# Optimization experiments

Hardware: AMD Instinct MI355X
Metric: run time of the kernel (lower is better)

Reference implementation:

```python
import jax, jax.numpy as jnp
import numpy as np
from jax import lax

D_IN, HIDDEN, B, T = 64, 512, 256, 256


def _lstm_layer(x, W_ih, W_hh, b_ih, b_hh):
    """PyTorch-convention LSTM layer. x: [B, T, in]. Returns (ys [B,T,H], h_last [B,H]).
    Gate order i, f, g, o; gates = x W_ih^T + h W_hh^T + b_ih + b_hh."""
    Bb = x.shape[0]
    H = W_hh.shape[1]
    # precompute input projection for all timesteps: [T, B, 4H]
    xg = jnp.einsum('bti,gi->tbg', x, W_ih) + (b_ih + b_hh)
    h0 = jnp.zeros((Bb, H), dtype=x.dtype)
    c0 = jnp.zeros((Bb, H), dtype=x.dtype)

    def step(carry, xg_t):
        h, c = carry
        gates = xg_t + h @ W_hh.T  # [B, 4H]
        i, f, g, o = jnp.split(gates, 4, axis=-1)
        i = jax.nn.sigmoid(i)
        f = jax.nn.sigmoid(f)
        g = jnp.tanh(g)
        o = jax.nn.sigmoid(o)
        c = f * c + i * g
        h = o * jnp.tanh(c)
        return (h, c), h

    (h_last, _), ys = lax.scan(step, (h0, c0), xg)
    return ys.transpose(1, 0, 2), h_last


def setup_inputs() -> dict:
    key = jax.random.key(0)
    ks = jax.random.split(key, 12)
    s0 = 1.0 / np.sqrt(HIDDEN)  # PyTorch default init scale
    u = lambda k, shp: jax.random.uniform(k, shp, jnp.float32, -s0, s0)
    return {
        'x': jax.random.normal(ks[0], (B, T, D_IN), jnp.float32),
        'W_ih0': u(ks[1], (4 * HIDDEN, D_IN)),
        'W_hh0': u(ks[2], (4 * HIDDEN, HIDDEN)),
        'b_ih0': u(ks[3], (4 * HIDDEN,)),
        'b_hh0': u(ks[4], (4 * HIDDEN,)),
        'W_ih1': u(ks[5], (4 * HIDDEN, HIDDEN)),
        'W_hh1': u(ks[6], (4 * HIDDEN, HIDDEN)),
        'b_ih1': u(ks[7], (4 * HIDDEN,)),
        'b_hh1': u(ks[8], (4 * HIDDEN,)),
        'head_w': u(ks[9], (1, HIDDEN)),
        'head_b': u(ks[10], (1,)),
    }


def reference(x, W_ih0, W_hh0, b_ih0, b_hh0, W_ih1, W_hh1, b_ih1, b_hh1, head_w, head_b):
    ys0, _ = _lstm_layer(x, W_ih0, W_hh0, b_ih0, b_hh0)          # [B, T, H]
    _, h_last = _lstm_layer(ys0, W_ih1, W_hh1, b_ih1, b_hh1)    # only last step used
    out = h_last @ head_w.T + head_b                              # [B, 1]
    return out[:, 0]                                              # squeeze(-1) -> [B]
```

## Files before the change

### kernel.cpp

```cpp
#include <hip/hip_runtime.h>

#define HID 512
#define NB  256
#define TT  256
#define DIN 64
#define HBUF 131072
#define SLOT_SH HBUF
#define NSLOT 8

typedef __attribute__((ext_vector_type(8))) short short8;
typedef __attribute__((ext_vector_type(4))) float f32x4;

__device__ __forceinline__ unsigned short f2bf(float f) {
    unsigned int u = __float_as_uint(f);
    u += 0x7FFF + ((u >> 16) & 1);
    return (unsigned short)(u >> 16);
}
__device__ __forceinline__ float bf2f(unsigned short h) {
    return __uint_as_float(((unsigned int)h) << 16);
}

__device__ __forceinline__ float fsig(float x) {
    return __builtin_amdgcn_rcpf(1.f + __expf(-x));
}
__device__ __forceinline__ float ftanh(float x) {
    return 1.f - 2.f * __builtin_amdgcn_rcpf(1.f + __expf(2.f * x));
}

__device__ __forceinline__ void st_u32_llc(unsigned* p, unsigned v) {
    asm volatile("global_store_dword %0, %1, off sc0 sc1" :: "v"(p), "v"(v) : "memory");
}
__device__ __forceinline__ unsigned ld_u32_llc(const unsigned* p) {
    unsigned v;
    asm volatile("global_load_dword %0, %1, off sc0 sc1\n\ts_waitcnt vmcnt(0)"
                 : "=v"(v) : "v"(p) : "memory");
    return v;
}

#define MFMA2(acc, a, bh, bl)                                               \
    acc = __builtin_amdgcn_mfma_f32_16x16x32_bf16(a, bh, acc, 0, 0, 0);     \
    acc = __builtin_amdgcn_mfma_f32_16x16x32_bf16(a, bl, acc, 0, 0, 0);
#define MFMA3(acc, ah, al, bh, bl)                                          \
    acc = __builtin_amdgcn_mfma_f32_16x16x32_bf16(ah, bh, acc, 0, 0, 0);    \
    acc = __builtin_amdgcn_mfma_f32_16x16x32_bf16(ah, bl, acc, 0, 0, 0);    \
    acc = __builtin_amdgcn_mfma_f32_16x16x32_bf16(al, bh, acc, 0, 0, 0);

#define SW0_N 9216
#define SW1_N 16384
#define LDS_BYTES ((SW0_N * 2 + SW1_N * 2) * 2)

__device__ __forceinline__ void store_h_pair(unsigned short* buf, size_t hoff,
                                             unsigned short v, int l) {
    unsigned int hv = (unsigned int)v;
    unsigned int up = __shfl_down(hv, 1);
    if ((l & 1) == 0)
        st_u32_llc((unsigned*)(buf + hoff), hv | (up << 16));
}

__device__ __forceinline__ void flag_wait(unsigned* fset, int target) {
    if (threadIdx.x < 128) {
        unsigned* p = fset + threadIdx.x;
        while ((int)ld_u32_llc(p) < target) __builtin_amdgcn_s_sleep(1);
    }
    __syncthreads();
}

__device__ __forceinline__ void orbit_transpose(f32x4& v, int m) {
    { float a = (m & 1) ? v[0] : v[1]; float b = __shfl_xor(a, 4); if (m & 1) v[0] = b; else v[1] = b; }
    { float a = (m & 1) ? v[2] : v[3]; float b = __shfl_xor(a, 4); if (m & 1) v[2] = b; else v[3] = b; }
    { float a = (m & 2) ? v[0] : v[2]; float b = __shfl_xor(a, 8); if (m & 2) v[0] = b; else v[2] = b; }
    { float a = (m & 2) ? v[1] : v[3]; float b = __shfl_xor(a, 8); if (m & 2) v[1] = b; else v[3] = b; }
}

__global__ __launch_bounds__(512, 2) void lstm_persistent(
    const float* __restrict__ x,
    const float* __restrict__ Wih0, const float* __restrict__ Whh0,
    const float* __restrict__ bih0, const float* __restrict__ bhh0,
    const float* __restrict__ Wih1, const float* __restrict__ Whh1,
    const float* __restrict__ bih1, const float* __restrict__ bhh1,
    const float* __restrict__ headw, const float* __restrict__ headb,
    unsigned short* h0base, unsigned short* h1base,
    unsigned* gf, float* __restrict__ out)
{
    extern __shared__ unsigned short lds[];
    unsigned short* sW0h = lds;
    unsigned short* sW0l = sW0h + SW0_N;
    unsigned short* sW1h = sW0l + SW0_N;
    unsigned short* sW1l = sW1h + SW1_N;

    const int tid = threadIdx.x;
    const int l   = tid & 63;
    const int w   = tid >> 6;
    const int bid = blockIdx.x;
    const int g   = bid & 1;
    const int jb  = bid >> 1;

    unsigned* f0g = gf + g * 128;
    unsigned* f1g = gf + 256 + g * 128;

    const int r  = l & 15;
    const int ks = (l >> 4) * 8;
    const int n  = (r >> 2) * HID + jb * 4 + (r & 3);
    {
        for (int kt = w; kt < 18; kt += 8) {
            const float* src = (kt < 2) ? (Wih0 + (size_t)n * DIN + kt * 32 + ks)
                                        : (Whh0 + (size_t)n * HID + (kt - 2) * 32 + ks);
            float v[8];
            *(float4*)&v[0] = *(const float4*)src;
            *(float4*)&v[4] = *(const float4*)(src + 4);
            union { unsigned short u[8]; uint4 q; } ph, pl;
            #pragma unroll
            for (int e = 0; e < 8; ++e) {
                unsigned short h = f2bf(v[e]);
                ph.u[e] = h; pl.u[e] = f2bf(v[e] - bf2f(h));
            }
            *(uint4*)&sW0h[(kt * 64 + l) * 8] = ph.q;
            *(uint4*)&sW0l[(kt * 64 + l) * 8] = pl.q;
        }
        for (int kt = w; kt < 32; kt += 8) {
            const float* src = (kt < 16) ? (Wih1 + (size_t)n * HID + kt * 32 + ks)
                                         : (Whh1 + (size_t)n * HID + (kt - 16) * 32 + ks);
            float v[8];
            *(float4*)&v[0] = *(const float4*)src;
            *(float4*)&v[4] = *(const float4*)(src + 4);
            union { unsigned short u[8]; uint4 q; } ph, pl;
            #pragma unroll
            for (int e = 0; e < 8; ++e) {
                unsigned short h = f2bf(v[e]);
                ph.u[e] = h; pl.u[e] = f2bf(v[e] - bf2f(h));
            }
            *(uint4*)&sW1h[(kt * 64 + l) * 8] = ph.q;
            *(uint4*)&sW1l[(kt * 64 + l) * 8] = pl.q;
        }
    }

    float bias0[4], bias1[4];
    #pragma unroll
    for (int gi = 0; gi < 4; ++gi) {
        const int nn = gi * HID + jb * 4 + (l & 3);
        bias0[gi] = bih0[nn] + bhh0[nn];
        bias1[gi] = bih1[nn] + bhh1[nn];
    }
    float c0 = 0.f, c1 = 0.f;

    const int m      = (l >> 2) & 3;
    const int b_in   = (l >> 4) * 4 + m;
    const int b_loc  = w * 16 + b_in;
    const int b_glob = g * 128 + b_loc;
    const int j_glob = jb * 4 + (l & 3);
    const size_t hoff = ((((size_t)(b_glob >> 4)) * 16 + (j_glob >> 5)) * 64
                         + ((b_glob & 15) | (((j_glob >> 3) & 3) << 4))) * 8 + (j_glob & 7);
    const int bt = g * 8 + w;

    const int xrow = g * 128 + w * 16 + (l & 15);
    float xv0[8], xv1[8];
    {
        const float* s0 = x + ((size_t)xrow * TT + 0) * DIN + ks;
        *(float4*)&xv0[0] = *(const float4*)s0;
        *(float4*)&xv0[4] = *(const float4*)(s0 + 4);
        *(float4*)&xv1[0] = *(const float4*)(s0 + 32);
        *(float4*)&xv1[4] = *(const float4*)(s0 + 36);
    }

    __syncthreads();

    const short8 bx0h = *(const short8*)&sW0h[(0 * 64 + l) * 8];
    const short8 bx0l = *(const short8*)&sW0l[(0 * 64 + l) * 8];
    const short8 bx1h = *(const short8*)&sW0h[(1 * 64 + l) * 8];
    const short8 bx1l = *(const short8*)&sW0l[(1 * 64 + l) * 8];

    for (int it = 0; it <= TT; ++it) {
        flag_wait(f0g, it);

        const unsigned short* h0c = h0base + (size_t)((it + 7) & 7) * SLOT_SH;
        unsigned short* h0n       = h0base + (size_t)(it & 7) * SLOT_SH;
        const unsigned short* h1c = h1base + (size_t)((it + 6) & 7) * SLOT_SH;
        unsigned short* h1n       = h1base + (size_t)((it + 7) & 7) * SLOT_SH;

        f32x4 acc0[2] = {{0.f,0.f,0.f,0.f},{0.f,0.f,0.f,0.f}};
        f32x4 acc1[2] = {{0.f,0.f,0.f,0.f},{0.f,0.f,0.f,0.f}};

        short8 fAh[16];
        #pragma unroll
        for (int kt = 0; kt < 16; ++kt) {
            const size_t o = (((size_t)bt * 16 + kt) * 64 + l) * 8;
            fAh[kt] = *(const short8*)&h0c[o];
        }

        if (it < TT) {
            {
                union { unsigned short u[8]; short8 s; } ah, al;
                #pragma unroll
                for (int e = 0; e < 8; ++e) {
                    unsigned short h = f2bf(xv0[e]);
                    ah.u[e] = h; al.u[e] = f2bf(xv0[e] - bf2f(h));
                }
                MFMA3(acc0[0], ah.s, al.s, bx0h, bx0l);
                #pragma unroll
                for (int e = 0; e < 8; ++e) {
                    unsigned short h = f2bf(xv1[e]);
                    ah.u[e] = h; al.u[e] = f2bf(xv1[e] - bf2f(h));
                }
                MFMA3(acc0[1], ah.s, al.s, bx1h, bx1l);
            }
            #pragma unroll
            for (int kt = 0; kt < 16; ++kt) {
                short8 bh = *(const short8*)&sW0h[((kt + 2) * 64 + l) * 8];
                short8 bl = *(const short8*)&sW0l[((kt + 2) * 64 + l) * 8];
                MFMA2(acc0[kt & 1], fAh[kt], bh, bl);
            }
            {
                f32x4 v = acc0[0] + acc0[1];
                orbit_transpose(v, m);
                const float iG = fsig(v[0] + bias0[0]);
                const float fG = fsig(v[1] + bias0[1]);
                const float gT = ftanh(v[2] + bias0[2]);
                const float oG = fsig(v[3] + bias0[3]);
                c0 = fmaf(fG, c0, iG * gT);
                const float h = oG * ftanh(c0);
                store_h_pair(h0n, hoff, f2bf(h), l);
            }
            asm volatile("s_waitcnt vmcnt(0)" ::: "memory");
            __syncthreads();
            if (tid == 0) st_u32_llc(f0g + jb, (unsigned)(it + 1));
        }

        if (it + 1 < TT) {
            const float* s0 = x + ((size_t)xrow * TT + (it + 1)) * DIN + ks;
            *(float4*)&xv0[0] = *(const float4*)s0;
            *(float4*)&xv0[4] = *(const float4*)(s0 + 4);
            *(float4*)&xv1[0] = *(const float4*)(s0 + 32);
            *(float4*)&xv1[4] = *(const float4*)(s0 + 36);
        }

        if (it > 0) {
            #pragma unroll
            for (int kt = 0; kt < 16; ++kt) {
                short8 bh = *(const short8*)&sW1h[(kt * 64 + l) * 8];
                short8 bl = *(const short8*)&sW1l[(kt * 64 + l) * 8];
                MFMA2(acc1[kt & 1], fAh[kt], bh, bl);
            }
        }

        flag_wait(f1g, it);

        if (it > 0) {
            short8 fCh[16];
            #pragma unroll
            for (int kt = 0; kt < 16; ++kt) {
                const size_t o = (((size_t)bt * 16 + kt) * 64 + l) * 8;
                fCh[kt] = *(const short8*)&h1c[o];
            }
            #pragma unroll
            for (int kt = 0; kt < 16; ++kt) {
                short8 bh = *(const short8*)&sW1h[((kt + 16) * 64 + l) * 8];
                short8 bl = *(const short8*)&sW1l[((kt + 16) * 64 + l) * 8];
                MFMA2(acc1[kt & 1], fCh[kt], bh, bl);
            }
            {
                f32x4 v = acc1[0] + acc1[1];
                orbit_transpose(v, m);
                const float iG = fsig(v[0] + bias1[0]);
                const float fG = fsig(v[1] + bias1[1]);
                const float gT = ftanh(v[2] + bias1[2]);
                const float oG = fsig(v[3] + bias1[3]);
                c1 = fmaf(fG, c1, iG * gT);
                const float h = oG * ftanh(c1);
                store_h_pair(h1n, hoff, f2bf(h), l);
            }
        }
        asm volatile("s_waitcnt vmcnt(0)" ::: "memory");
        __syncthreads();
        if (tid == 0) st_u32_llc(f1g + jb, (unsigned)(it + 1));
        if ((it & 7) == 7 && tid >= 448)
            __builtin_amdgcn_fence(__ATOMIC_ACQUIRE, "agent");
    }

    if (jb == 0) {
        if (tid < 128) {
            unsigned* p = f1g + tid;
            while ((int)ld_u32_llc(p) < TT + 1) __builtin_amdgcn_s_sleep(1);
        }
        __syncthreads();
        const unsigned short* h1h = h1base + (size_t)((TT + 7) & 7) * SLOT_SH;
        const int bl_ = tid >> 2;
        const int qd  = tid & 3;
        const int b   = g * 128 + bl_;
        const int btw = b >> 4;
        float s = 0.f;
        #pragma unroll
        for (int jt = qd * 4; jt < qd * 4 + 4; ++jt) {
            #pragma unroll
            for (int q2 = 0; q2 < 4; ++q2) {
                const size_t off = (((size_t)btw * 16 + jt) * 64 + ((b & 15) | (q2 << 4))) * 8;
                short8 vh = *(const short8*)&h1h[off];
                const int j0 = jt * 32 + q2 * 8;
                #pragma unroll
                for (int e = 0; e < 8; ++e)
                    s += bf2f((unsigned short)vh[e]) * headw[j0 + e];
            }
        }
        s += __shfl_down(s, 2, 4);
        s += __shfl_down(s, 1, 4);
        if (qd == 0) out[b] = s + headb[0];
    }
}

extern "C" void kernel_launch(void* const* d_in, const int* in_sizes, int n_in,
                              void* d_out, int out_size, void* d_ws, size_t ws_size,
                              hipStream_t stream) {
    const float* x      = (const float*)d_in[0];
    const float* W_ih0  = (const float*)d_in[1];
    const float* W_hh0  = (const float*)d_in[2];
    const float* b_ih0  = (const float*)d_in[3];
    const float* b_hh0  = (const float*)d_in[4];
    const float* W_ih1  = (const float*)d_in[5];
    const float* W_hh1  = (const float*)d_in[6];
    const float* b_ih1  = (const float*)d_in[7];
    const float* b_hh1  = (const float*)d_in[8];
    const float* head_w = (const float*)d_in[9];
    const float* head_b = (const float*)d_in[10];
    float* out = (float*)d_out;

    const size_t SLOT_BYTES = (size_t)SLOT_SH * 2;
    unsigned* gf = (unsigned*)d_ws;
    unsigned short* h0base = (unsigned short*)((char*)d_ws + (1 << 20));
    unsigned short* h1base = (unsigned short*)((char*)d_ws + (1 << 20) + NSLOT * SLOT_BYTES);

    hipMemsetAsync(d_ws, 0, 4096, stream);
    hipMemsetAsync((char*)h0base + 7 * SLOT_BYTES, 0, SLOT_BYTES, stream);
    hipMemsetAsync((char*)h1base + 7 * SLOT_BYTES, 0, SLOT_BYTES, stream);

    hipFuncSetAttribute((const void*)lstm_persistent,
                        hipFuncAttributeMaxDynamicSharedMemorySize, LDS_BYTES);
    lstm_persistent<<<dim3(256), dim3(512), LDS_BYTES, stream>>>(
        x, W_ih0, W_hh0, b_ih0, b_hh0, W_ih1, W_hh1, b_ih1, b_hh1,
        head_w, head_b, h0base, h1base, gf, out);
}
```

Before: 1.803 ms.

## Drop low-part weight split and repartition blocks into four batch groups

Stores the weights as a single bf16 copy instead of a hi/lo split pair. This removes one MFMA per weight tile and halves the LDS weight reads, at the cost of weight precision. It also re-partitions the grid into four batch groups of 64 with eight hidden units per block, two waves per batch tile, which shrinks the flag set each block polls from 128 to 64. The head reduction is adjusted to match the new batch-group size.

```diff
diff --git a/kernel.cpp b/kernel.cpp
--- a/kernel.cpp
+++ b/kernel.cpp
@@ -37,17 +37,13 @@
     return v;
 }
 
-#define MFMA2(acc, a, bh, bl)                                               \
-    acc = __builtin_amdgcn_mfma_f32_16x16x32_bf16(a, bh, acc, 0, 0, 0);     \
-    acc = __builtin_amdgcn_mfma_f32_16x16x32_bf16(a, bl, acc, 0, 0, 0);
-#define MFMA3(acc, ah, al, bh, bl)                                          \
-    acc = __builtin_amdgcn_mfma_f32_16x16x32_bf16(ah, bh, acc, 0, 0, 0);    \
-    acc = __builtin_amdgcn_mfma_f32_16x16x32_bf16(ah, bl, acc, 0, 0, 0);    \
-    acc = __builtin_amdgcn_mfma_f32_16x16x32_bf16(al, bh, acc, 0, 0, 0);
-
-#define SW0_N 9216
-#define SW1_N 16384
-#define LDS_BYTES ((SW0_N * 2 + SW1_N * 2) * 2)
+#define MFMA1(acc, a, b) acc = __builtin_amdgcn_mfma_f32_16x16x32_bf16(a, b, acc, 0, 0, 0)
+
+#define SW0_F 36
+#define SW1_F 64
+#define SW0_N (SW0_F * 512)
+#define SW1_N (SW1_F * 512)
+#define LDS_BYTES ((SW0_N + SW1_N) * 2)
 
 __device__ __forceinline__ void store_h_pair(unsigned short* buf, size_t hoff,
                                              unsigned short v, int l) {
@@ -58,7 +54,7 @@
 }
 
 __device__ __forceinline__ void flag_wait(unsigned* fset, int target) {
-    if (threadIdx.x < 128) {
+    if (threadIdx.x < 64) {
         unsigned* p = fset + threadIdx.x;
         while ((int)ld_u32_llc(p) < target) __builtin_amdgcn_s_sleep(1);
     }
@@ -83,61 +79,57 @@
     unsigned* gf, float* __restrict__ out)
 {
     extern __shared__ unsigned short lds[];
-    unsigned short* sW0h = lds;
-    unsigned short* sW0l = sW0h + SW0_N;
-    unsigned short* sW1h = sW0l + SW0_N;
-    unsigned short* sW1l = sW1h + SW1_N;
+    unsigned short* sW0 = lds;
+    unsigned short* sW1 = lds + SW0_N;
 
     const int tid = threadIdx.x;
     const int l   = tid & 63;
     const int w   = tid >> 6;
+    const int bt  = w >> 1;
+    const int bf  = w & 1;
     const int bid = blockIdx.x;
-    const int g   = bid & 1;
-    const int jb  = bid >> 1;
-
-    unsigned* f0g = gf + g * 128;
-    unsigned* f1g = gf + 256 + g * 128;
-
-    const int r  = l & 15;
-    const int ks = (l >> 4) * 8;
-    const int n  = (r >> 2) * HID + jb * 4 + (r & 3);
+    const int gq  = bid & 3;
+    const int jb  = bid >> 2;
+
+    unsigned* f0g = gf + gq * 64;
+    unsigned* f1g = gf + 256 + gq * 64;
+
+    const int r16 = l & 15;
+    const int ko  = (l >> 4) * 8;
     {
-        for (int kt = w; kt < 18; kt += 8) {
-            const float* src = (kt < 2) ? (Wih0 + (size_t)n * DIN + kt * 32 + ks)
-                                        : (Whh0 + (size_t)n * HID + (kt - 2) * 32 + ks);
+        const int nrow = (r16 >> 2) * HID + jb * 8 + (r16 & 3);
+        for (int fi = w; fi < SW0_F; fi += 8) {
+            const int kt = fi >> 1, bf_ = fi & 1;
+            const int n = nrow + bf_ * 4;
+            const float* src = (kt < 2) ? (Wih0 + (size_t)n * DIN + kt * 32 + ko)
+                                        : (Whh0 + (size_t)n * HID + (kt - 2) * 32 + ko);
             float v[8];
             *(float4*)&v[0] = *(const float4*)src;
             *(float4*)&v[4] = *(const float4*)(src + 4);
-            union { unsigned short u[8]; uint4 q; } ph, pl;
-            #pragma unroll
-            for (int e = 0; e < 8; ++e) {
-                unsigned short h = f2bf(v[e]);
-                ph.u[e] = h; pl.u[e] = f2bf(v[e] - bf2f(h));
-            }
-            *(uint4*)&sW0h[(kt * 64 + l) * 8] = ph.q;
-            *(uint4*)&sW0l[(kt * 64 + l) * 8] = pl.q;
-        }
-        for (int kt = w; kt < 32; kt += 8) {
-            const float* src = (kt < 16) ? (Wih1 + (size_t)n * HID + kt * 32 + ks)
-                                         : (Whh1 + (size_t)n * HID + (kt - 16) * 32 + ks);
+            union { unsigned short u[8]; uint4 q; } pb;
+            #pragma unroll
+            for (int e = 0; e < 8; ++e) pb.u[e] = f2bf(v[e]);
+            *(uint4*)&sW0[fi * 512 + l * 8] = pb.q;
+        }
+        for (int fi = w; fi < SW1_F; fi += 8) {
+            const int kt = fi >> 1, bf_ = fi & 1;
+            const int n = nrow + bf_ * 4;
+            const float* src = (kt < 16) ? (Wih1 + (size_t)n * HID + kt * 32 + ko)
+                                         : (Whh1 + (size_t)n * HID + (kt - 16) * 32 + ko);
             float v[8];
             *(float4*)&v[0] = *(const float4*)src;
             *(float4*)&v[4] = *(const float4*)(src + 4);
-            union { unsigned short u[8]; uint4 q; } ph, pl;
-            #pragma unroll
-            for (int e = 0; e < 8; ++e) {
-                unsigned short h = f2bf(v[e]);
-                ph.u[e] = h; pl.u[e] = f2bf(v[e] - bf2f(h));
-            }
-            *(uint4*)&sW1h[(kt * 64 + l) * 8] = ph.q;
-            *(uint4*)&sW1l[(kt * 64 + l) * 8] = pl.q;
+            union { unsigned short u[8]; uint4 q; } pb;
+            #pragma unroll
+            for (int e = 0; e < 8; ++e) pb.u[e] = f2bf(v[e]);
+            *(uint4*)&sW1[fi * 512 + l * 8] = pb.q;
         }
     }
 
     float bias0[4], bias1[4];
     #pragma unroll
     for (int gi = 0; gi < 4; ++gi) {
-        const int nn = gi * HID + jb * 4 + (l & 3);
+        const int nn = gi * HID + jb * 8 + bf * 4 + (l & 3);
         bias0[gi] = bih0[nn] + bhh0[nn];
         bias1[gi] = bih1[nn] + bhh1[nn];
     }
@@ -145,17 +137,16 @@
 
     const int m      = (l >> 2) & 3;
     const int b_in   = (l >> 4) * 4 + m;
-    const int b_loc  = w * 16 + b_in;
-    const int b_glob = g * 128 + b_loc;
-    const int j_glob = jb * 4 + (l & 3);
+    const int b_glob = gq * 64 + bt * 16 + b_in;
+    const int j_glob = jb * 8 + bf * 4 + (l & 3);
     const size_t hoff = ((((size_t)(b_glob >> 4)) * 16 + (j_glob >> 5)) * 64
                          + ((b_glob & 15) | (((j_glob >> 3) & 3) << 4))) * 8 + (j_glob & 7);
-    const int bt = g * 8 + w;
-
-    const int xrow = g * 128 + w * 16 + (l & 15);
+    const int btg = gq * 4 + bt;
+
+    const int xrow = gq * 64 + bt * 16 + (l & 15);
     float xv0[8], xv1[8];
     {
-        const float* s0 = x + ((size_t)xrow * TT + 0) * DIN + ks;
+        const float* s0 = x + ((size_t)xrow * TT + 0) * DIN + ko;
         *(float4*)&xv0[0] = *(const float4*)s0;
         *(float4*)&xv0[4] = *(const float4*)(s0 + 4);
         *(float4*)&xv1[0] = *(const float4*)(s0 + 32);
@@ -164,10 +155,8 @@
 
     __syncthreads();
 
-    const short8 bx0h = *(const short8*)&sW0h[(0 * 64 + l) * 8];
-    const short8 bx0l = *(const short8*)&sW0l[(0 * 64 + l) * 8];
-    const short8 bx1h = *(const short8*)&sW0h[(1 * 64 + l) * 8];
-    const short8 bx1l = *(const short8*)&sW0l[(1 * 64 + l) * 8];
+    const short8 bx0 = *(const short8*)&sW0[(0 * 2 + bf) * 512 + l * 8];
+    const short8 bx1 = *(const short8*)&sW0[(1 * 2 + bf) * 512 + l * 8];
 
     for (int it = 0; it <= TT; ++it) {
         flag_wait(f0g, it);
@@ -183,7 +172,7 @@
         short8 fAh[16];
         #pragma unroll
         for (int kt = 0; kt < 16; ++kt) {
-            const size_t o = (((size_t)bt * 16 + kt) * 64 + l) * 8;
+            const size_t o = (((size_t)btg * 16 + kt) * 64 + l) * 8;
             fAh[kt] = *(const short8*)&h0c[o];
         }
 
@@ -195,19 +184,20 @@
                     unsigned short h = f2bf(xv0[e]);
                     ah.u[e] = h; al.u[e] = f2bf(xv0[e] - bf2f(h));
                 }
-                MFMA3(acc0[0], ah.s, al.s, bx0h, bx0l);
+                MFMA1(acc0[0], ah.s, bx0);
+                MFMA1(acc0[0], al.s, bx0);
                 #pragma unroll
                 for (int e = 0; e < 8; ++e) {
                     unsigned short h = f2bf(xv1[e]);
                     ah.u[e] = h; al.u[e] = f2bf(xv1[e] - bf2f(h));
                 }
-                MFMA3(acc0[1], ah.s, al.s, bx1h, bx1l);
+                MFMA1(acc0[1], ah.s, bx1);
+                MFMA1(acc0[1], al.s, bx1);
             }
             #pragma unroll
             for (int kt = 0; kt < 16; ++kt) {
-                short8 bh = *(const short8*)&sW0h[((kt + 2) * 64 + l) * 8];
-                short8 bl = *(const short8*)&sW0l[((kt + 2) * 64 + l) * 8];
-                MFMA2(acc0[kt & 1], fAh[kt], bh, bl);
+                short8 b = *(const short8*)&sW0[((kt + 2) * 2 + bf) * 512 + l * 8];
+                MFMA1(acc0[kt & 1], fAh[kt], b);
             }
             {
                 f32x4 v = acc0[0] + acc0[1];
@@ -226,7 +216,7 @@
         }
 
         if (it + 1 < TT) {
-            const float* s0 = x + ((size_t)xrow * TT + (it + 1)) * DIN + ks;
+            const float* s0 = x + ((size_t)xrow * TT + (it + 1)) * DIN + ko;
             *(float4*)&xv0[0] = *(const float4*)s0;
             *(float4*)&xv0[4] = *(const float4*)(s0 + 4);
             *(float4*)&xv1[0] = *(const float4*)(s0 + 32);
@@ -236,9 +226,8 @@
         if (it > 0) {
             #pragma unroll
             for (int kt = 0; kt < 16; ++kt) {
-                short8 bh = *(const short8*)&sW1h[(kt * 64 + l) * 8];
-                short8 bl = *(const short8*)&sW1l[(kt * 64 + l) * 8];
-                MFMA2(acc1[kt & 1], fAh[kt], bh, bl);
+                short8 b = *(const short8*)&sW1[(kt * 2 + bf) * 512 + l * 8];
+                MFMA1(acc1[kt & 1], fAh[kt], b);
             }
         }
 
@@ -248,14 +237,13 @@
             short8 fCh[16];
             #pragma unroll
             for (int kt = 0; kt < 16; ++kt) {
-                const size_t o = (((size_t)bt * 16 + kt) * 64 + l) * 8;
+                const size_t o = (((size_t)btg * 16 + kt) * 64 + l) * 8;
                 fCh[kt] = *(const short8*)&h1c[o];
             }
             #pragma unroll
             for (int kt = 0; kt < 16; ++kt) {
-                short8 bh = *(const short8*)&sW1h[((kt + 16) * 64 + l) * 8];
-                short8 bl = *(const short8*)&sW1l[((kt + 16) * 64 + l) * 8];
-                MFMA2(acc1[kt & 1], fCh[kt], bh, bl);
+                short8 b = *(const short8*)&sW1[((16 + kt) * 2 + bf) * 512 + l * 8];
+                MFMA1(acc1[kt & 1], fCh[kt], b);
             }
             {
                 f32x4 v = acc1[0] + acc1[1];
@@ -277,19 +265,19 @@
     }
 
     if (jb == 0) {
-        if (tid < 128) {
+        if (tid < 64) {
             unsigned* p = f1g + tid;
             while ((int)ld_u32_llc(p) < TT + 1) __builtin_amdgcn_s_sleep(1);
         }
         __syncthreads();
         const unsigned short* h1h = h1base + (size_t)((TT + 7) & 7) * SLOT_SH;
-        const int bl_ = tid >> 2;
-        const int qd  = tid & 3;
-        const int b   = g * 128 + bl_;
+        const int bl_ = tid >> 3;
+        const int qd  = tid & 7;
+        const int b   = gq * 64 + bl_;
         const int btw = b >> 4;
         float s = 0.f;
         #pragma unroll
-        for (int jt = qd * 4; jt < qd * 4 + 4; ++jt) {
+        for (int jt = qd * 2; jt < qd * 2 + 2; ++jt) {
             #pragma unroll
             for (int q2 = 0; q2 < 4; ++q2) {
                 const size_t off = (((size_t)btw * 16 + jt) * 64 + ((b & 15) | (q2 << 4))) * 8;
@@ -300,8 +288,9 @@
                     s += bf2f((unsigned short)vh[e]) * headw[j0 + e];
             }
         }
-        s += __shfl_down(s, 2, 4);
-        s += __shfl_down(s, 1, 4);
+        s += __shfl_down(s, 4, 8);
+        s += __shfl_down(s, 2, 8);
+        s += __shfl_down(s, 1, 8);
         if (qd == 0) out[b] = s + headb[0];
     }
 }
```

Result: faster. 1.450 ms, median of 3 (-19.6%).
